# Kernel optimization log

Hardware: AMD Instinct MI355X
Metric: run time of the kernel (lower is better)

## Reference

```python
import jax, jax.numpy as jnp
import numpy as np

B, LQ, LK, D = 8, 2048, 2048, 128

def setup_inputs() -> dict:
    key = jax.random.key(0)
    k1, k2, k3, k4 = jax.random.split(key, 4)
    return {
        "query": jax.random.normal(k1, (B, LQ, D), dtype=jnp.float32),
        "key": jax.random.normal(k2, (B, LK, D), dtype=jnp.float32),
        "value": jax.random.normal(k3, (B, LK, D), dtype=jnp.float32),
        "scale_factor": jax.random.normal(k4, (B, LQ, LK), dtype=jnp.float32),
    }

def reference(query, key, value, scale_factor):
    # qk: [B, LQ, LK]
    qk = jnp.einsum("bqd,bkd->bqk", query, key)
    probs = jax.nn.softmax(qk * scale_factor, axis=-1)
    # dropout_p = 0.0 -> identity
    return jnp.einsum("bqk,bkd->bqd", probs, value)
```

## Files before the change

kernel.cpp:

```cpp
#include <hip/hip_runtime.h>
#include <hip/hip_bf16.h>


typedef float          f32x4 __attribute__((ext_vector_type(4)));
typedef short          s16x8 __attribute__((ext_vector_type(8)));
typedef unsigned int   u32x4 __attribute__((ext_vector_type(4)));
typedef unsigned short u16x4 __attribute__((ext_vector_type(4)));

#define LOG2E 1.4426950408889634f

__device__ __forceinline__ float fast_exp2(float x) {
#if __has_builtin(__builtin_amdgcn_exp2f)
    return __builtin_amdgcn_exp2f(x);
#else
    return exp2f(x);
#endif
}

__device__ __forceinline__ unsigned short f2bf(float x) {
    return __builtin_bit_cast(unsigned short, __float2bfloat16(x));
}
__device__ __forceinline__ float bf2f(unsigned short u) {
    return __bfloat162float(__builtin_bit_cast(__hip_bfloat16, u));
}

__global__ void prep(const float* __restrict__ q,
                     const float* __restrict__ k,
                     const float* __restrict__ v,
                     unsigned short* __restrict__ qh,
                     unsigned short* __restrict__ ql,
                     unsigned short* __restrict__ kh,
                     unsigned short* __restrict__ kl,
                     unsigned short* __restrict__ vt) {
    __shared__ unsigned short tile[64 * 132];
    const int bb  = blockIdx.x;
    const int tid = threadIdx.x;

    if (bb < 4096) {
        const bool isq = bb < 2048;
        const float* src = isq ? q : k;
        unsigned short* hi = isq ? qh : kh;
        unsigned short* lo = isq ? ql : kl;
        const int i = (isq ? bb : bb - 2048) * 256 + tid;
        const float4 val = ((const float4*)src)[i];
        float f[4] = {val.x, val.y, val.z, val.w};
        u16x4 h, l;
#pragma unroll
        for (int j = 0; j < 4; ++j) {
            unsigned short hb = f2bf(f[j]);
            h[j] = hb;
            l[j] = f2bf(f[j] - bf2f(hb));
        }
        ((u16x4*)hi)[i] = h;
        ((u16x4*)lo)[i] = l;
        return;
    }

    const int tb = bb - 4096;
    const int b  = tb & 7;
    const int k0 = (tb >> 3) * 64;
#pragma unroll
    for (int p = 0; p < 8; ++p) {
        int idx  = p * 256 + tid;
        int kk   = idx >> 5;
        int dblk = idx & 31;
        float4 val = ((const float4*)v)[((b * 2048 + k0 + kk) * 128 + dblk * 4) >> 2];
        u16x4 t4;
        t4[0] = f2bf(val.x); t4[1] = f2bf(val.y);
        t4[2] = f2bf(val.z); t4[3] = f2bf(val.w);
        *(u16x4*)&tile[kk * 132 + dblk * 4] = t4;
    }
    __syncthreads();
#pragma unroll
    for (int p = 0; p < 4; ++p) {
        int idx = p * 256 + tid;
        int d   = idx >> 3;
        int k8  = idx & 7;
        u16x4 a, c;
#pragma unroll
        for (int j = 0; j < 4; ++j) a[j] = tile[(k8 * 8 + j) * 132 + d];
#pragma unroll
        for (int j = 0; j < 4; ++j) c[j] = tile[(k8 * 8 + 4 + j) * 132 + d];
        unsigned short* outp = vt + (b * 128 + d) * 2048 + k0 + k8 * 8;
        *(u16x4*)outp       = a;
        *(u16x4*)(outp + 4) = c;
    }
}

#define KHS 136
#define PS  72

__global__ __launch_bounds__(256, 3)
void flash_fwd(const unsigned short* __restrict__ qh_g,
               const unsigned short* __restrict__ ql_g,
               const unsigned short* __restrict__ kh_g,
               const unsigned short* __restrict__ kl_g,
               const unsigned short* __restrict__ vt_g,
               const float* __restrict__ scale_g,
               float* __restrict__ opart,
               float* __restrict__ mpart,
               float* __restrict__ lpart) {
    __shared__ unsigned short lds_kh[64 * KHS];
    __shared__ unsigned short lds_kl[64 * KHS];
    __shared__ unsigned short lds_p[4][16 * PS];

    const int tid  = threadIdx.x;
    const int wave = tid >> 6;
    const int lane = tid & 63;
    const int c    = lane & 15;
    const int g    = lane >> 4;

    const int bid   = blockIdx.x;
    const int b     = bid & 7;
    const int qt    = (bid >> 3) & 31;
    const int ks    = bid >> 8;
    const int q0    = qt * 64;
    const int kbase = ks * 1024;

    const int srow = tid >> 4, sc8 = tid & 15;

    s16x8 qh[4], ql[4];
    {
        const int qrow = b * 2048 + q0 + wave * 16 + c;
#pragma unroll
        for (int kstep = 0; kstep < 4; ++kstep) {
            int idx = qrow * 16 + kstep * 4 + g;
            qh[kstep] = __builtin_bit_cast(s16x8, ((const u32x4*)qh_g)[idx]);
            ql[kstep] = __builtin_bit_cast(s16x8, ((const u32x4*)ql_g)[idx]);
        }
    }

    f32x4 oacc[8];
#pragma unroll
    for (int t = 0; t < 8; ++t) oacc[t] = (f32x4){0.f, 0.f, 0.f, 0.f};
    float m2[4], ln[4];
#pragma unroll
    for (int r = 0; r < 4; ++r) { m2[r] = -INFINITY; ln[r] = 0.f; }

    u32x4 pk[4], pl[4];
    float scn[4][4];
    const int scb = (b * 2048 + q0 + wave * 16 + g * 4) * 2048 + c;

    {
        const int k0 = kbase;
#pragma unroll
        for (int p = 0; p < 4; ++p) {
            int gidx = (b * 2048 + k0 + p * 16 + srow) * 16 + sc8;
            pk[p] = ((const u32x4*)kh_g)[gidx];
            pl[p] = ((const u32x4*)kl_g)[gidx];
        }
#pragma unroll
        for (int t = 0; t < 4; ++t)
#pragma unroll
            for (int r = 0; r < 4; ++r)
                scn[t][r] = scale_g[scb + r * 2048 + k0 + t * 16];
    }

    for (int kc = 0; kc < 16; ++kc) {
        const int k0 = kbase + kc * 64;

        __syncthreads();
#pragma unroll
        for (int p = 0; p < 4; ++p) {
            *(u32x4*)&lds_kh[(p * 16 + srow) * KHS + sc8 * 8] = pk[p];
            *(u32x4*)&lds_kl[(p * 16 + srow) * KHS + sc8 * 8] = pl[p];
        }
        __syncthreads();

        float sc[4][4];
#pragma unroll
        for (int t = 0; t < 4; ++t)
#pragma unroll
            for (int r = 0; r < 4; ++r)
                sc[t][r] = scn[t][r] * LOG2E;

        if (kc < 15) {
            const int kn = k0 + 64;
#pragma unroll
            for (int p = 0; p < 4; ++p) {
                int gidx = (b * 2048 + kn + p * 16 + srow) * 16 + sc8;
                pk[p] = ((const u32x4*)kh_g)[gidx];
                pl[p] = ((const u32x4*)kl_g)[gidx];
            }
#pragma unroll
            for (int t = 0; t < 4; ++t)
#pragma unroll
                for (int r = 0; r < 4; ++r)
                    scn[t][r] = scale_g[scb + r * 2048 + kn + t * 16];
        }

        f32x4 s[4];
#pragma unroll
        for (int t = 0; t < 4; ++t) s[t] = (f32x4){0.f, 0.f, 0.f, 0.f};
#pragma unroll
        for (int kstep = 0; kstep < 4; ++kstep) {
#pragma unroll
            for (int t = 0; t < 4; ++t) {
                int off = (t * 16 + c) * KHS + kstep * 32 + g * 8;
                s16x8 bh = *(const s16x8*)&lds_kh[off];
                s16x8 bl = *(const s16x8*)&lds_kl[off];
                s[t] = __builtin_amdgcn_mfma_f32_16x16x32_bf16(qh[kstep], bh, s[t], 0, 0, 0);
                s[t] = __builtin_amdgcn_mfma_f32_16x16x32_bf16(ql[kstep], bh, s[t], 0, 0, 0);
                s[t] = __builtin_amdgcn_mfma_f32_16x16x32_bf16(qh[kstep], bl, s[t], 0, 0, 0);
            }
        }

        float lt[4][4], mx[4];
#pragma unroll
        for (int r = 0; r < 4; ++r) {
            lt[0][r] = s[0][r] * sc[0][r];
            lt[1][r] = s[1][r] * sc[1][r];
            lt[2][r] = s[2][r] * sc[2][r];
            lt[3][r] = s[3][r] * sc[3][r];
            mx[r] = fmaxf(fmaxf(lt[0][r], lt[1][r]), fmaxf(lt[2][r], lt[3][r]));
        }
#pragma unroll
        for (int mask = 1; mask < 16; mask <<= 1)
#pragma unroll
            for (int r = 0; r < 4; ++r)
                mx[r] = fmaxf(mx[r], __shfl_xor(mx[r], mask));
        float al[4], rs[4];
#pragma unroll
        for (int r = 0; r < 4; ++r) {
            float mn = fmaxf(m2[r], mx[r]);
            al[r] = fast_exp2(m2[r] - mn);
            m2[r] = mn;
            rs[r] = 0.f;
        }
#pragma unroll
        for (int t = 0; t < 4; ++t)
#pragma unroll
            for (int r = 0; r < 4; ++r) {
                float p = fast_exp2(lt[t][r] - m2[r]);
                rs[r] += p;
                lds_p[wave][(g * 4 + r) * PS + t * 16 + c] = f2bf(p);
            }
#pragma unroll
        for (int mask = 1; mask < 16; mask <<= 1)
#pragma unroll
            for (int r = 0; r < 4; ++r)
                rs[r] += __shfl_xor(rs[r], mask);
#pragma unroll
        for (int r = 0; r < 4; ++r) ln[r] = ln[r] * al[r] + rs[r];
#pragma unroll
        for (int t = 0; t < 8; ++t)
#pragma unroll
            for (int r = 0; r < 4; ++r) oacc[t][r] *= al[r];

#pragma unroll
        for (int k2 = 0; k2 < 2; ++k2) {
            s16x8 af = *(const s16x8*)&lds_p[wave][c * PS + k2 * 32 + g * 8];
            const int vb = (b * 128 + c) * 256 + (k0 >> 3) + k2 * 4 + g;
            s16x8 bv[8];
#pragma unroll
            for (int t2 = 0; t2 < 8; ++t2)
                bv[t2] = __builtin_bit_cast(s16x8, ((const u32x4*)vt_g)[vb + t2 * 4096]);
#pragma unroll
            for (int t2 = 0; t2 < 8; ++t2)
                oacc[t2] = __builtin_amdgcn_mfma_f32_16x16x32_bf16(af, bv[t2], oacc[t2], 0, 0, 0);
        }
    }

    {
        const int rowb = (ks * 8 + b) * 2048 + q0 + wave * 16;
#pragma unroll
        for (int t2 = 0; t2 < 8; ++t2)
#pragma unroll
            for (int r = 0; r < 4; ++r)
                opart[(rowb + g * 4 + r) * 128 + t2 * 16 + c] = oacc[t2][r];
        if (c == 0) {
#pragma unroll
            for (int r = 0; r < 4; ++r) {
                mpart[rowb + g * 4 + r] = m2[r];
                lpart[rowb + g * 4 + r] = ln[r];
            }
        }
    }
}

__global__ void merge_halves(const float* __restrict__ opart,
                             const float* __restrict__ mpart,
                             const float* __restrict__ lpart,
                             float* __restrict__ out) {
    const int row = blockIdx.x;
    const int d   = threadIdx.x;
    const float m0 = mpart[row],  m1 = mpart[16384 + row];
    const float l0 = lpart[row],  l1 = lpart[16384 + row];
    const float M  = fmaxf(m0, m1);
    const float a0 = fast_exp2(m0 - M);
    const float a1 = fast_exp2(m1 - M);
    const float inv = 1.f / (a0 * l0 + a1 * l1);
    const int i = row * 128 + d;
    out[i] = (a0 * opart[i] + a1 * opart[16384 * 128 + i]) * inv;
}

extern "C" void kernel_launch(void* const* d_in, const int* in_sizes, int n_in,
                              void* d_out, int out_size, void* d_ws, size_t ws_size,
                              hipStream_t stream) {
    const float* q  = (const float*)d_in[0];
    const float* k  = (const float*)d_in[1];
    const float* v  = (const float*)d_in[2];
    const float* sc = (const float*)d_in[3];
    float* out = (float*)d_out;

    char* ws = (char*)d_ws;
    const size_t MB = 1024 * 1024;
    unsigned short* qh = (unsigned short*)(ws);
    unsigned short* ql = (unsigned short*)(ws + 4 * MB);
    unsigned short* kh = (unsigned short*)(ws + 8 * MB);
    unsigned short* kl = (unsigned short*)(ws + 12 * MB);
    unsigned short* vt = (unsigned short*)(ws + 16 * MB);
    float* opart = (float*)(ws + 20 * MB);
    float* mpart = (float*)(ws + 36 * MB);
    float* lpart = (float*)(ws + 36 * MB + 128 * 1024);

    prep<<<4352, 256, 0, stream>>>(q, k, v, qh, ql, kh, kl, vt);
    flash_fwd<<<512, 256, 0, stream>>>(qh, ql, kh, kl, vt, sc, opart, mpart, lpart);
    merge_halves<<<16384, 128, 0, stream>>>(opart, mpart, lpart, out);
}
```

Measured before the change: 298.9 us.

## Split keys four ways, stage V tiles in LDS, shrink key chunk to 32

The flash kernel is templated on the key-split count, and a 4-way split is launched when the workspace is large enough, doubling the grid to 1024 blocks. Each iteration now processes 32 keys instead of 64. V^T tiles are staged through LDS with a register prefetch rather than read directly from global memory inside the PV loop, and launch bounds rise to 4 blocks per SM. The merge kernel is generalised to combine KSPLIT partial results. This trades more partial-output traffic and merge work, plus more iterations and barriers per key, for better occupancy and coalesced V loads.

```diff
diff --git a/kernel.cpp b/kernel.cpp
--- a/kernel.cpp
+++ b/kernel.cpp
@@ -88,9 +88,11 @@
 }
 
 #define KHS 136
-#define PS  72
-
-__global__ __launch_bounds__(256, 3)
+#define VTS 40
+#define PS  40
+
+template <int KSPLIT>
+__global__ __launch_bounds__(256, 4)
 void flash_fwd(const unsigned short* __restrict__ qh_g,
                const unsigned short* __restrict__ ql_g,
                const unsigned short* __restrict__ kh_g,
@@ -100,8 +102,9 @@
                float* __restrict__ opart,
                float* __restrict__ mpart,
                float* __restrict__ lpart) {
-    __shared__ unsigned short lds_kh[64 * KHS];
-    __shared__ unsigned short lds_kl[64 * KHS];
+    __shared__ unsigned short lds_kh[32 * KHS];
+    __shared__ unsigned short lds_kl[32 * KHS];
+    __shared__ unsigned short lds_vt[128 * VTS];
     __shared__ unsigned short lds_p[4][16 * PS];
 
     const int tid  = threadIdx.x;
@@ -115,9 +118,11 @@
     const int qt    = (bid >> 3) & 31;
     const int ks    = bid >> 8;
     const int q0    = qt * 64;
-    const int kbase = ks * 1024;
+    const int kbase = ks * (2048 / KSPLIT);
+    const int NIT   = 2048 / KSPLIT / 32;
 
     const int srow = tid >> 4, sc8 = tid & 15;
+    const int sdv  = tid >> 2, sk4 = tid & 3;
 
     s16x8 qh[4], ql[4];
     {
@@ -137,65 +142,70 @@
 #pragma unroll
     for (int r = 0; r < 4; ++r) { m2[r] = -INFINITY; ln[r] = 0.f; }
 
-    u32x4 pk[4], pl[4];
-    float scn[4][4];
+    u32x4 pk[2], pl[2], pv[2];
+    float scn[2][4];
     const int scb = (b * 2048 + q0 + wave * 16 + g * 4) * 2048 + c;
 
     {
         const int k0 = kbase;
 #pragma unroll
-        for (int p = 0; p < 4; ++p) {
+        for (int p = 0; p < 2; ++p) {
             int gidx = (b * 2048 + k0 + p * 16 + srow) * 16 + sc8;
             pk[p] = ((const u32x4*)kh_g)[gidx];
             pl[p] = ((const u32x4*)kl_g)[gidx];
-        }
-#pragma unroll
-        for (int t = 0; t < 4; ++t)
+            int vidx = (b * 128 + p * 64 + sdv) * 256 + (k0 >> 3) + sk4;
+            pv[p] = ((const u32x4*)vt_g)[vidx];
+        }
+#pragma unroll
+        for (int t = 0; t < 2; ++t)
 #pragma unroll
             for (int r = 0; r < 4; ++r)
                 scn[t][r] = scale_g[scb + r * 2048 + k0 + t * 16];
     }
 
-    for (int kc = 0; kc < 16; ++kc) {
-        const int k0 = kbase + kc * 64;
+    for (int kc = 0; kc < NIT; ++kc) {
+        const int k0 = kbase + kc * 32;
 
         __syncthreads();
 #pragma unroll
-        for (int p = 0; p < 4; ++p) {
+        for (int p = 0; p < 2; ++p) {
             *(u32x4*)&lds_kh[(p * 16 + srow) * KHS + sc8 * 8] = pk[p];
             *(u32x4*)&lds_kl[(p * 16 + srow) * KHS + sc8 * 8] = pl[p];
+            *(u32x4*)&lds_vt[(p * 64 + sdv) * VTS + sk4 * 8]  = pv[p];
         }
         __syncthreads();
 
-        float sc[4][4];
-#pragma unroll
-        for (int t = 0; t < 4; ++t)
+        float sc[2][4];
+#pragma unroll
+        for (int t = 0; t < 2; ++t)
 #pragma unroll
             for (int r = 0; r < 4; ++r)
                 sc[t][r] = scn[t][r] * LOG2E;
 
-        if (kc < 15) {
-            const int kn = k0 + 64;
-#pragma unroll
-            for (int p = 0; p < 4; ++p) {
+        if (kc < NIT - 1) {
+            const int kn = k0 + 32;
+#pragma unroll
+            for (int p = 0; p < 2; ++p) {
                 int gidx = (b * 2048 + kn + p * 16 + srow) * 16 + sc8;
                 pk[p] = ((const u32x4*)kh_g)[gidx];
                 pl[p] = ((const u32x4*)kl_g)[gidx];
-            }
-#pragma unroll
-            for (int t = 0; t < 4; ++t)
+                int vidx = (b * 128 + p * 64 + sdv) * 256 + (kn >> 3) + sk4;
+                pv[p] = ((const u32x4*)vt_g)[vidx];
+            }
+#pragma unroll
+            for (int t = 0; t < 2; ++t)
 #pragma unroll
                 for (int r = 0; r < 4; ++r)
                     scn[t][r] = scale_g[scb + r * 2048 + kn + t * 16];
         }
 
-        f32x4 s[4];
-#pragma unroll
-        for (int t = 0; t < 4; ++t) s[t] = (f32x4){0.f, 0.f, 0.f, 0.f};
+        f32x4 s[2];
+#pragma unroll
+        for (int t = 0; t < 2; ++t) s[t] = (f32x4){0.f, 0.f, 0.f, 0.f};
 #pragma unroll
         for (int kstep = 0; kstep < 4; ++kstep) {
 #pragma unroll
-            for (int t = 0; t < 4; ++t) {
+            for (int t = 0; t < 2; ++t) {
                 int off = (t * 16 + c) * KHS + kstep * 32 + g * 8;
                 s16x8 bh = *(const s16x8*)&lds_kh[off];
                 s16x8 bl = *(const s16x8*)&lds_kl[off];
@@ -205,14 +215,12 @@
             }
         }
 
-        float lt[4][4], mx[4];
+        float lt[2][4], mx[4];
 #pragma unroll
         for (int r = 0; r < 4; ++r) {
             lt[0][r] = s[0][r] * sc[0][r];
             lt[1][r] = s[1][r] * sc[1][r];
-            lt[2][r] = s[2][r] * sc[2][r];
-            lt[3][r] = s[3][r] * sc[3][r];
-            mx[r] = fmaxf(fmaxf(lt[0][r], lt[1][r]), fmaxf(lt[2][r], lt[3][r]));
+            mx[r] = fmaxf(lt[0][r], lt[1][r]);
         }
 #pragma unroll
         for (int mask = 1; mask < 16; mask <<= 1)
@@ -228,7 +236,7 @@
             rs[r] = 0.f;
         }
 #pragma unroll
-        for (int t = 0; t < 4; ++t)
+        for (int t = 0; t < 2; ++t)
 #pragma unroll
             for (int r = 0; r < 4; ++r) {
                 float p = fast_exp2(lt[t][r] - m2[r]);
@@ -247,17 +255,13 @@
 #pragma unroll
             for (int r = 0; r < 4; ++r) oacc[t][r] *= al[r];
 
-#pragma unroll
-        for (int k2 = 0; k2 < 2; ++k2) {
-            s16x8 af = *(const s16x8*)&lds_p[wave][c * PS + k2 * 32 + g * 8];
-            const int vb = (b * 128 + c) * 256 + (k0 >> 3) + k2 * 4 + g;
-            s16x8 bv[8];
-#pragma unroll
-            for (int t2 = 0; t2 < 8; ++t2)
-                bv[t2] = __builtin_bit_cast(s16x8, ((const u32x4*)vt_g)[vb + t2 * 4096]);
-#pragma unroll
-            for (int t2 = 0; t2 < 8; ++t2)
-                oacc[t2] = __builtin_amdgcn_mfma_f32_16x16x32_bf16(af, bv[t2], oacc[t2], 0, 0, 0);
+        {
+            s16x8 af = *(const s16x8*)&lds_p[wave][c * PS + g * 8];
+#pragma unroll
+            for (int t2 = 0; t2 < 8; ++t2) {
+                s16x8 bv = *(const s16x8*)&lds_vt[(t2 * 16 + c) * VTS + g * 8];
+                oacc[t2] = __builtin_amdgcn_mfma_f32_16x16x32_bf16(af, bv, oacc[t2], 0, 0, 0);
+            }
         }
     }
 
@@ -267,7 +271,7 @@
         for (int t2 = 0; t2 < 8; ++t2)
 #pragma unroll
             for (int r = 0; r < 4; ++r)
-                opart[(rowb + g * 4 + r) * 128 + t2 * 16 + c] = oacc[t2][r];
+                opart[(size_t)(rowb + g * 4 + r) * 128 + t2 * 16 + c] = oacc[t2][r];
         if (c == 0) {
 #pragma unroll
             for (int r = 0; r < 4; ++r) {
@@ -278,20 +282,30 @@
     }
 }
 
-__global__ void merge_halves(const float* __restrict__ opart,
-                             const float* __restrict__ mpart,
-                             const float* __restrict__ lpart,
-                             float* __restrict__ out) {
+template <int KSPLIT>
+__global__ void merge_parts(const float* __restrict__ opart,
+                            const float* __restrict__ mpart,
+                            const float* __restrict__ lpart,
+                            float* __restrict__ out) {
     const int row = blockIdx.x;
     const int d   = threadIdx.x;
-    const float m0 = mpart[row],  m1 = mpart[16384 + row];
-    const float l0 = lpart[row],  l1 = lpart[16384 + row];
-    const float M  = fmaxf(m0, m1);
-    const float a0 = fast_exp2(m0 - M);
-    const float a1 = fast_exp2(m1 - M);
-    const float inv = 1.f / (a0 * l0 + a1 * l1);
-    const int i = row * 128 + d;
-    out[i] = (a0 * opart[i] + a1 * opart[16384 * 128 + i]) * inv;
+    float m[KSPLIT], l[KSPLIT];
+    float M = -INFINITY;
+#pragma unroll
+    for (int i = 0; i < KSPLIT; ++i) {
+        m[i] = mpart[i * 16384 + row];
+        l[i] = lpart[i * 16384 + row];
+        M = fmaxf(M, m[i]);
+    }
+    float denom = 0.f, acc = 0.f;
+    const size_t base = (size_t)row * 128 + d;
+#pragma unroll
+    for (int i = 0; i < KSPLIT; ++i) {
+        const float a = fast_exp2(m[i] - M);
+        denom += a * l[i];
+        acc   += a * opart[(size_t)i * 16384 * 128 + base];
+    }
+    out[base] = acc / denom;
 }
 
 extern "C" void kernel_launch(void* const* d_in, const int* in_sizes, int n_in,
@@ -310,11 +324,21 @@
     unsigned short* kh = (unsigned short*)(ws + 8 * MB);
     unsigned short* kl = (unsigned short*)(ws + 12 * MB);
     unsigned short* vt = (unsigned short*)(ws + 16 * MB);
-    float* opart = (float*)(ws + 20 * MB);
-    float* mpart = (float*)(ws + 36 * MB);
-    float* lpart = (float*)(ws + 36 * MB + 128 * 1024);
 
     prep<<<4352, 256, 0, stream>>>(q, k, v, qh, ql, kh, kl, vt);
-    flash_fwd<<<512, 256, 0, stream>>>(qh, ql, kh, kl, vt, sc, opart, mpart, lpart);
-    merge_halves<<<16384, 128, 0, stream>>>(opart, mpart, lpart, out);
-}
+
+    const size_t need4 = 20 * MB + (size_t)4 * 16384 * 128 * 4 + (size_t)2 * 4 * 16384 * 4;
+    if (ws_size >= need4) {
+        float* opart = (float*)(ws + 20 * MB);
+        float* mpart = (float*)(ws + 52 * MB);
+        float* lpart = (float*)(ws + 52 * MB + 256 * 1024);
+        flash_fwd<4><<<1024, 256, 0, stream>>>(qh, ql, kh, kl, vt, sc, opart, mpart, lpart);
+        merge_parts<4><<<16384, 128, 0, stream>>>(opart, mpart, lpart, out);
+    } else {
+        float* opart = (float*)(ws + 20 * MB);
+        float* mpart = (float*)(ws + 36 * MB);
+        float* lpart = (float*)(ws + 36 * MB + 128 * 1024);
+        flash_fwd<2><<<512, 256, 0, stream>>>(qh, ql, kh, kl, vt, sc, opart, mpart, lpart);
+        merge_parts<2><<<16384, 128, 0, stream>>>(opart, mpart, lpart, out);
+    }
+}
```

After: 271.2 us. 1.1x faster.
